# Kernel optimization log

Measured on AMD Instinct MI355X. Metric: run time of the kernel, lower is better.

## Reference

```python
import jax, jax.numpy as jnp
import numpy as np

TEMPERATURE = 0.5
N_NODES = 100000
N_EDGES = 3200000
D = 32


def setup_inputs() -> dict:
    key = jax.random.key(0)
    ks = jax.random.split(key, 8)
    node_reps = jax.random.normal(ks[0], (N_NODES, D), dtype=jnp.float32)
    edge_reps = jax.random.normal(ks[1], (N_EDGES, D), dtype=jnp.float32)
    graph_rep = jax.random.normal(ks[2], (D,), dtype=jnp.float32)
    subgraph_rep = jax.random.normal(ks[3], (D,), dtype=jnp.float32)
    W = jax.random.normal(ks[4], (3 * D, D), dtype=jnp.float32) / np.sqrt(3 * D)
    b = jax.random.normal(ks[5], (D,), dtype=jnp.float32) * 0.01
    edge_index = jax.random.randint(ks[6], (2, N_EDGES), 0, N_NODES, dtype=jnp.int64)
    selection = jax.random.randint(ks[7], (N_EDGES,), 0, 2) > 0
    return {
        "node_reps": node_reps,
        "edge_reps": edge_reps,
        "graph_rep": graph_rep,
        "subgraph_rep": subgraph_rep,
        "W": W,
        "b": b,
        "edge_index": edge_index,
        "selection": selection,
    }


def reference(node_reps, edge_reps, graph_rep, subgraph_rep, W, b, edge_index, selection):
    # Gather endpoint node reps per edge: [E, 32] each
    src = node_reps[edge_index[0]]
    dst = node_reps[edge_index[1]]
    # Concat -> [E, 96], Linear + ELU -> [E, 32]
    h = jnp.concatenate([src, dst, edge_reps], axis=1)
    edge_action_reps = jax.nn.elu(h @ W + b)
    # State scores: [E] = [E,32] @ [32]
    state_prob = edge_action_reps @ (graph_rep - subgraph_rep)
    # Mask already-selected edges to the global minimum, then softmax with temperature
    min_prob = jnp.min(state_prob)
    state_prob = jnp.where(selection, min_prob, state_prob)
    return jax.nn.softmax(state_prob[None, :] / TEMPERATURE, axis=1)
```

## Files before the change

### kernel.cpp

```cpp
#include <hip/hip_runtime.h>
#include <hip/hip_bf16.h>
#include <stdint.h>

#define DD 32
#define KH 96


typedef __attribute__((ext_vector_type(16))) float vf16;

__device__ __forceinline__ uint32_t fkey(float f) {
    uint32_t b = __float_as_uint(f);
    return (b & 0x80000000u) ? ~b : (b | 0x80000000u);
}
__device__ __forceinline__ float funkey(uint32_t k) {
    uint32_t b = (k & 0x80000000u) ? (k & 0x7FFFFFFFu) : ~k;
    return __uint_as_float(b);
}
__device__ __forceinline__ float bflo(uint32_t w) { return __uint_as_float(w << 16); }
__device__ __forceinline__ float bfhi(uint32_t w) { return __uint_as_float(w & 0xFFFF0000u); }
__device__ __forceinline__ uint16_t f2bf(float v) {
    uint32_t u = __float_as_uint(v);
    uint32_t r = (u + 0x7FFFu + ((u >> 16) & 1u)) >> 16;
    return (uint16_t)r;
}

__device__ __forceinline__ void wload(const float* p, vf16& a, vf16& b) {
    asm volatile("s_load_dwordx16 %0, %2, 0x0\n\t"
                 "s_load_dwordx16 %1, %2, 0x40\n\t"
                 "s_waitcnt lgkmcnt(0)"
                 : "=&s"(a), "=&s"(b)
                 : "s"(p));
}

__global__ void k_init(const void* W, const void* bias, const void* g, const void* sg,
                       const void* ei, const void* sel,
                       uint32_t* hdr, float* Wf, float* bf, float* vf, int E, int N) {
    int t = threadIdx.x;
    __shared__ int sh_i32, sh_gt1, sh_odd, sh_f32;
    if (t == 0) { sh_i32 = 0; sh_gt1 = 0; sh_odd = 0; sh_f32 = 0; }
    __syncthreads();

    const uint16_t* wb = (const uint16_t*)W;
    for (int i = t; i < KH * DD; i += 256) {
        float x = bflo((uint32_t)wb[i]);
        if (!(fabsf(x) < 1e4f)) sh_f32 = 1;
    }
    const long long* ell = (const long long*)ei;
    int ns = 2048 < E ? 2048 : E;
    for (int i = t; i < ns; i += 256) {
        long long v = ell[i];
        if (v < 0 || v >= (long long)N) sh_i32 = 1;
    }
    const uint32_t* sw = (const uint32_t*)sel;
    int ns2 = 2048 < E / 4 ? 2048 : E / 4;
    for (int i = t; i < ns2; i += 256) {
        uint32_t v = sw[i];
        if (v > 1u) sh_gt1 = 1;
        if (v != 0u && (i & 1)) sh_odd = 1;
    }
    __syncthreads();
    int fmode = sh_f32;

    for (int i = t; i < KH * DD; i += 256)
        Wf[i] = fmode ? ((const float*)W)[i] : bflo((uint32_t)wb[i]);
    for (int i = t; i < DD; i += 256) {
        bf[i] = fmode ? ((const float*)bias)[i] : bflo((uint32_t)((const uint16_t*)bias)[i]);
        float gv = fmode ? ((const float*)g)[i]  : bflo((uint32_t)((const uint16_t*)g)[i]);
        float sv = fmode ? ((const float*)sg)[i] : bflo((uint32_t)((const uint16_t*)sg)[i]);
        vf[i] = gv - sv;
    }
    if (t == 0) {
        hdr[0] = (uint32_t)sh_i32;
        hdr[1] = sh_gt1 ? 2u : (sh_odd ? 1u : 0u);
        hdr[2] = (uint32_t)fmode;
        hdr[3] = 0xFFFFFFFFu;
        hdr[4] = 0u;
        hdr[5] = 0u;
        hdr[6] = 0u;
    }
}

__device__ __forceinline__ void loadrow(const char* __restrict__ p, int fmode, float* h) {
    if (fmode) {
        const float4* q = (const float4*)p;
        #pragma unroll
        for (int t = 0; t < 8; ++t) {
            float4 u = q[t];
            h[t * 4 + 0] = u.x; h[t * 4 + 1] = u.y; h[t * 4 + 2] = u.z; h[t * 4 + 3] = u.w;
        }
    } else {
        const uint4* q = (const uint4*)p;
        #pragma unroll
        for (int t = 0; t < 4; ++t) {
            uint4 u = q[t];
            h[t * 8 + 0] = bflo(u.x); h[t * 8 + 1] = bfhi(u.x);
            h[t * 8 + 2] = bflo(u.y); h[t * 8 + 3] = bfhi(u.y);
            h[t * 8 + 4] = bflo(u.z); h[t * 8 + 5] = bfhi(u.z);
            h[t * 8 + 6] = bflo(u.w); h[t * 8 + 7] = bfhi(u.w);
        }
    }
}

__device__ __forceinline__ bool fetch_sel(const char* sel, int mode, int e) {
    if (mode == 2) return ((const uint8_t*)sel)[e] != 0;
    if (mode == 1) return ((const int*)sel)[e] != 0;
    return ((const long long*)sel)[e] != 0;
}

__device__ __forceinline__ void sp_store(float* __restrict__ ws_sp, void* __restrict__ out,
                                         int use_ws, int fmode, int e, float v) {
    if (use_ws) ws_sp[e] = v;
    else if (fmode) ((float*)out)[e] = v;
    else ((uint16_t*)out)[e] = f2bf(v);
}
__device__ __forceinline__ float sp_load(const float* __restrict__ ws_sp, const void* __restrict__ out,
                                         int use_ws, int fmode, int e) {
    if (use_ws) return ws_sp[e];
    if (fmode) return ((const float*)out)[e];
    return bflo((uint32_t)((const uint16_t*)out)[e]);
}

__global__ __launch_bounds__(256) void k_pass1(
    const char* __restrict__ node, const char* __restrict__ edgep,
    const char* __restrict__ ei, const char* __restrict__ sel,
    uint32_t* __restrict__ hdr, const float* __restrict__ Wf,
    const float* __restrict__ bf, const float* __restrict__ vf,
    float* __restrict__ ws_sp, void* __restrict__ out,
    int use_ws, int E, int N) {
    const int idx_mode = (int)hdr[0];
    const int sel_mode = (int)hdr[1];
    const int fmode    = (int)hdr[2];

    int e = blockIdx.x * 256 + threadIdx.x;
    bool valid = e < E;
    int ec = valid ? e : E - 1;

    long long si, di;
    if (idx_mode) { si = ((const int*)ei)[ec]; di = ((const int*)ei)[E + ec]; }
    else          { si = ((const long long*)ei)[ec]; di = ((const long long*)ei)[(size_t)E + ec]; }
    int s0 = (int)si; s0 = s0 < 0 ? 0 : (s0 >= N ? N - 1 : s0);
    int d0 = (int)di; d0 = d0 < 0 ? 0 : (d0 >= N ? N - 1 : d0);

    size_t rb = fmode ? 128 : 64;
    const char* p0 = node  + (size_t)s0 * rb;
    const char* p1 = node  + (size_t)d0 * rb;
    const char* p2 = edgep + (size_t)ec * rb;

    float acc[DD];
    {
        vf16 b0, b1;
        wload(bf, b0, b1);
        #pragma unroll
        for (int j = 0; j < 16; ++j) { acc[j] = b0[j]; acc[16 + j] = b1[j]; }
    }

    float hh[32], hn[32];
    loadrow(p0, fmode, hh);

    #pragma unroll 1
    for (int r = 0; r < 3; ++r) {
        if (r < 2) {
            const char* pn = (r == 0) ? p1 : p2;
            loadrow(pn, fmode, hn);
        }
        const float* wp = Wf + r * 32 * DD;
        #pragma unroll
        for (int k = 0; k < 32; ++k) {
            vf16 w0, w1;
            wload(wp + k * DD, w0, w1);
            float hk = hh[k];
            #pragma unroll
            for (int j = 0; j < 16; ++j) {
                acc[j]      = fmaf(hk, w0[j], acc[j]);
                acc[16 + j] = fmaf(hk, w1[j], acc[16 + j]);
            }
        }
        if (r < 2) {
            #pragma unroll
            for (int k = 0; k < 32; ++k) hh[k] = hn[k];
        }
    }

    float sp = 0.f;
    {
        vf16 v0, v1;
        wload(vf, v0, v1);
        #pragma unroll
        for (int j = 0; j < 16; ++j) {
            float a = acc[j];
            float act = a > 0.f ? a : (__expf(a) - 1.f);
            sp = fmaf(act, v0[j], sp);
            float a2 = acc[16 + j];
            float act2 = a2 > 0.f ? a2 : (__expf(a2) - 1.f);
            sp = fmaf(act2, v1[j], sp);
        }
    }

    bool selv = true;
    if (valid) {
        sp_store(ws_sp, out, use_ws, fmode, e, sp);
        selv = fetch_sel(sel, sel_mode, e);
    }

    float mn = valid ? sp : __builtin_inff();
    float mx = (valid && !selv) ? sp : -__builtin_inff();
    uint32_t c = (valid && !selv) ? 1u : 0u;
    #pragma unroll
    for (int o = 32; o >= 1; o >>= 1) {
        mn = fminf(mn, __shfl_xor(mn, o));
        mx = fmaxf(mx, __shfl_xor(mx, o));
        c += __shfl_xor(c, o);
    }
    __shared__ float smn[4], smx[4];
    __shared__ uint32_t sc[4];
    int wid = threadIdx.x >> 6, lane = threadIdx.x & 63;
    if (lane == 0) { smn[wid] = mn; smx[wid] = mx; sc[wid] = c; }
    __syncthreads();
    if (threadIdx.x == 0) {
        for (int w = 1; w < 4; ++w) { mn = fminf(mn, smn[w]); mx = fmaxf(mx, smx[w]); c += sc[w]; }
        atomicMin(&hdr[3], fkey(mn));
        atomicMax(&hdr[4], fkey(mx));
        if (c) atomicAdd(&hdr[5], c);
    }
}

__global__ __launch_bounds__(256) void k_pass2(
    const char* __restrict__ sel, uint32_t* __restrict__ hdr,
    const float* __restrict__ ws_sp, const void* __restrict__ out,
    int use_ws, int E) {
    int e = blockIdx.x * 256 + threadIdx.x;
    int sel_mode = (int)hdr[1], fmode = (int)hdr[2];
    float mn = funkey(hdr[3]);
    uint32_t cnt = hdr[5];
    float M = cnt ? funkey(hdr[4]) : mn;
    float p = 0.f;
    if (e < E) {
        float sp = sp_load(ws_sp, out, use_ws, fmode, e);
        bool selv = fetch_sel(sel, sel_mode, e);
        float masked = selv ? mn : sp;
        p = __expf((masked - M) * 2.0f);
    }
    #pragma unroll
    for (int o = 32; o >= 1; o >>= 1) p += __shfl_xor(p, o);
    __shared__ float sps[4];
    int wid = threadIdx.x >> 6, lane = threadIdx.x & 63;
    if (lane == 0) sps[wid] = p;
    __syncthreads();
    if (threadIdx.x == 0) {
        p += sps[1] + sps[2] + sps[3];
        atomicAdd((float*)&hdr[6], p);
    }
}

__global__ __launch_bounds__(256) void k_pass3(
    const char* __restrict__ sel, const uint32_t* __restrict__ hdr,
    const float* __restrict__ ws_sp, void* __restrict__ out,
    int use_ws, int E) {
    int e = blockIdx.x * 256 + threadIdx.x;
    if (e >= E) return;
    int sel_mode = (int)hdr[1], fmode = (int)hdr[2];
    float mn = funkey(hdr[3]);
    uint32_t cnt = hdr[5];
    float M = cnt ? funkey(hdr[4]) : mn;
    float S = __uint_as_float(hdr[6]);
    float sp = sp_load(ws_sp, out, use_ws, fmode, e);
    bool selv = fetch_sel(sel, sel_mode, e);
    float masked = selv ? mn : sp;
    float r = __expf((masked - M) * 2.0f) / S;
    if (fmode) ((float*)out)[e] = r;
    else       ((uint16_t*)out)[e] = f2bf(r);
}

extern "C" void kernel_launch(void* const* d_in, const int* in_sizes, int n_in,
                              void* d_out, int out_size, void* d_ws, size_t ws_size,
                              hipStream_t stream) {
    int N = in_sizes[0] / DD;
    int E = in_sizes[1] / DD;
    const void* node = d_in[0];
    const void* edge = d_in[1];
    const void* g    = d_in[2];
    const void* sg   = d_in[3];
    const void* W    = d_in[4];
    const void* bias = d_in[5];
    const void* ei   = d_in[6];
    const void* sel  = d_in[7];

    uint8_t* ws = (uint8_t*)d_ws;
    uint32_t* hdr = (uint32_t*)ws;
    float* Wf = (float*)(ws + 256);
    float* bf = (float*)(ws + 256 + 12288);
    float* vf = (float*)(ws + 256 + 12288 + 128);
    float* sp_arr = (float*)(ws + 16384);
    int use_ws = (ws_size >= (size_t)16384 + (size_t)E * sizeof(float)) ? 1 : 0;

    int grid = (E + 255) / 256;
    k_init<<<1, 256, 0, stream>>>(W, bias, g, sg, ei, sel, hdr, Wf, bf, vf, E, N);
    k_pass1<<<grid, 256, 0, stream>>>((const char*)node, (const char*)edge, (const char*)ei,
                                      (const char*)sel, hdr, Wf, bf, vf, sp_arr, d_out,
                                      use_ws, E, N);
    k_pass2<<<grid, 256, 0, stream>>>((const char*)sel, hdr, sp_arr, d_out, use_ws, E);
    k_pass3<<<grid, 256, 0, stream>>>((const char*)sel, hdr, sp_arr, d_out, use_ws, E);
}
```

Measured before the change: 1.131 ms.

## Stream weights via vector loads with triple-buffer prefetch; grid-stride all passes

Swaps the scalar s_load weight fetches, each of which waited on its own load, for per-thread float4 vector loads of W. These are triple-buffered two rows ahead so the loads overlap the FMAs, which are written as explicit v_fmac inline asm. All three passes become grid-stride loops with capped grids (2048 blocks for pass1, 1024 for passes 2 and 3), which cuts the per-block atomics and reduction overhead. Launch bounds now ask for 2 blocks per SIMD. The risks are higher VGPR pressure from the 24 float4 weight registers, and redundant per-lane vector loads of data that is uniform across the wave.

```diff
diff --git a/kernel.cpp b/kernel.cpp
--- a/kernel.cpp
+++ b/kernel.cpp
@@ -5,8 +5,6 @@
 #define DD 32
 #define KH 96
 
-
-typedef __attribute__((ext_vector_type(16))) float vf16;
 
 __device__ __forceinline__ uint32_t fkey(float f) {
     uint32_t b = __float_as_uint(f);
@@ -24,13 +22,7 @@
     return (uint16_t)r;
 }
 
-__device__ __forceinline__ void wload(const float* p, vf16& a, vf16& b) {
-    asm volatile("s_load_dwordx16 %0, %2, 0x0\n\t"
-                 "s_load_dwordx16 %1, %2, 0x40\n\t"
-                 "s_waitcnt lgkmcnt(0)"
-                 : "=&s"(a), "=&s"(b)
-                 : "s"(p));
-}
+#define VFMAC(d, a, b) asm("v_fmac_f32 %0, %1, %2" : "+v"(d) : "v"(a), "v"(b))
 
 __global__ void k_init(const void* W, const void* bias, const void* g, const void* sg,
                        const void* ei, const void* sel,
@@ -120,7 +112,26 @@
     return bflo((uint32_t)((const uint16_t*)out)[e]);
 }
 
-__global__ __launch_bounds__(256) void k_pass1(
+#define RSEC(R)                                                             \
+    _Pragma("unroll")                                                       \
+    for (int k = 0; k < 32; ++k) {                                          \
+        const int g = (R) * 32 + k;                                         \
+        if (g + 2 < 96) {                                                   \
+            _Pragma("unroll")                                               \
+            for (int q = 0; q < 8; ++q) w[(g + 2) % 3][q] = wq[(g + 2) * 8 + q]; \
+        }                                                                   \
+        float hk = hh[k];                                                   \
+        _Pragma("unroll")                                                   \
+        for (int q = 0; q < 8; ++q) {                                       \
+            float4 c4 = w[g % 3][q];                                        \
+            VFMAC(acc[q * 4 + 0], hk, c4.x);                                \
+            VFMAC(acc[q * 4 + 1], hk, c4.y);                                \
+            VFMAC(acc[q * 4 + 2], hk, c4.z);                                \
+            VFMAC(acc[q * 4 + 3], hk, c4.w);                                \
+        }                                                                   \
+    }
+
+__global__ __launch_bounds__(256, 2) void k_pass1(
     const char* __restrict__ node, const char* __restrict__ edgep,
     const char* __restrict__ ei, const char* __restrict__ sel,
     uint32_t* __restrict__ hdr, const float* __restrict__ Wf,
@@ -131,80 +142,78 @@
     const int sel_mode = (int)hdr[1];
     const int fmode    = (int)hdr[2];
 
-    int e = blockIdx.x * 256 + threadIdx.x;
-    bool valid = e < E;
-    int ec = valid ? e : E - 1;
-
-    long long si, di;
-    if (idx_mode) { si = ((const int*)ei)[ec]; di = ((const int*)ei)[E + ec]; }
-    else          { si = ((const long long*)ei)[ec]; di = ((const long long*)ei)[(size_t)E + ec]; }
-    int s0 = (int)si; s0 = s0 < 0 ? 0 : (s0 >= N ? N - 1 : s0);
-    int d0 = (int)di; d0 = d0 < 0 ? 0 : (d0 >= N ? N - 1 : d0);
-
-    size_t rb = fmode ? 128 : 64;
-    const char* p0 = node  + (size_t)s0 * rb;
-    const char* p1 = node  + (size_t)d0 * rb;
-    const char* p2 = edgep + (size_t)ec * rb;
-
-    float acc[DD];
-    {
-        vf16 b0, b1;
-        wload(bf, b0, b1);
-        #pragma unroll
-        for (int j = 0; j < 16; ++j) { acc[j] = b0[j]; acc[16 + j] = b1[j]; }
-    }
-
-    float hh[32], hn[32];
-    loadrow(p0, fmode, hh);
-
-    #pragma unroll 1
-    for (int r = 0; r < 3; ++r) {
-        if (r < 2) {
-            const char* pn = (r == 0) ? p1 : p2;
-            loadrow(pn, fmode, hn);
-        }
-        const float* wp = Wf + r * 32 * DD;
-        #pragma unroll
-        for (int k = 0; k < 32; ++k) {
-            vf16 w0, w1;
-            wload(wp + k * DD, w0, w1);
-            float hk = hh[k];
-            #pragma unroll
-            for (int j = 0; j < 16; ++j) {
-                acc[j]      = fmaf(hk, w0[j], acc[j]);
-                acc[16 + j] = fmaf(hk, w1[j], acc[16 + j]);
-            }
-        }
-        if (r < 2) {
-            #pragma unroll
-            for (int k = 0; k < 32; ++k) hh[k] = hn[k];
-        }
-    }
-
-    float sp = 0.f;
-    {
-        vf16 v0, v1;
-        wload(vf, v0, v1);
+    const float4* __restrict__ wq = (const float4*)Wf;
+    const float4* __restrict__ bq = (const float4*)bf;
+    const float4* __restrict__ vq = (const float4*)vf;
+
+    float mnA = __builtin_inff();
+    float mxA = -__builtin_inff();
+    uint32_t cA = 0;
+
+    const int stride = gridDim.x * 256;
+    for (int e = blockIdx.x * 256 + threadIdx.x; e < E; e += stride) {
+        long long si, di;
+        if (idx_mode) { si = ((const int*)ei)[e]; di = ((const int*)ei)[E + e]; }
+        else          { si = ((const long long*)ei)[e]; di = ((const long long*)ei)[(size_t)E + e]; }
+        int s0 = (int)si; s0 = s0 < 0 ? 0 : (s0 >= N ? N - 1 : s0);
+        int d0 = (int)di; d0 = d0 < 0 ? 0 : (d0 >= N ? N - 1 : d0);
+
+        size_t rb = fmode ? 128 : 64;
+        const char* p0 = node  + (size_t)s0 * rb;
+        const char* p1 = node  + (size_t)d0 * rb;
+        const char* p2 = edgep + (size_t)e * rb;
+
+        float hh[DD];
+        loadrow(p0, fmode, hh);
+
+        float acc[DD];
+        #pragma unroll
+        for (int q = 0; q < 8; ++q) {
+            float4 b4 = bq[q];
+            acc[q * 4 + 0] = b4.x; acc[q * 4 + 1] = b4.y;
+            acc[q * 4 + 2] = b4.z; acc[q * 4 + 3] = b4.w;
+        }
+
+        float4 w[3][8];
+        #pragma unroll
+        for (int q = 0; q < 8; ++q) w[0][q] = wq[q];
+        #pragma unroll
+        for (int q = 0; q < 8; ++q) w[1][q] = wq[8 + q];
+
+        RSEC(0)
+        loadrow(p1, fmode, hh);
+        RSEC(1)
+        loadrow(p2, fmode, hh);
+        RSEC(2)
+
+        float vv[DD];
+        #pragma unroll
+        for (int q = 0; q < 8; ++q) {
+            float4 v4 = vq[q];
+            vv[q * 4 + 0] = v4.x; vv[q * 4 + 1] = v4.y;
+            vv[q * 4 + 2] = v4.z; vv[q * 4 + 3] = v4.w;
+        }
+        float sp = 0.f;
         #pragma unroll
         for (int j = 0; j < 16; ++j) {
             float a = acc[j];
             float act = a > 0.f ? a : (__expf(a) - 1.f);
-            sp = fmaf(act, v0[j], sp);
+            sp = fmaf(act, vv[j], sp);
             float a2 = acc[16 + j];
             float act2 = a2 > 0.f ? a2 : (__expf(a2) - 1.f);
-            sp = fmaf(act2, v1[j], sp);
-        }
-    }
-
-    bool selv = true;
-    if (valid) {
+            sp = fmaf(act2, vv[16 + j], sp);
+        }
+
         sp_store(ws_sp, out, use_ws, fmode, e, sp);
-        selv = fetch_sel(sel, sel_mode, e);
-    }
-
-    float mn = valid ? sp : __builtin_inff();
-    float mx = (valid && !selv) ? sp : -__builtin_inff();
-    uint32_t c = (valid && !selv) ? 1u : 0u;
+        bool selv = fetch_sel(sel, sel_mode, e);
+
+        mnA = fminf(mnA, sp);
+        mxA = selv ? mxA : fmaxf(mxA, sp);
+        cA += selv ? 0u : 1u;
+    }
+
+    float mn = mnA, mx = mxA;
+    uint32_t c = cA;
     #pragma unroll
     for (int o = 32; o >= 1; o >>= 1) {
         mn = fminf(mn, __shfl_xor(mn, o));
@@ -217,7 +226,7 @@
     if (lane == 0) { smn[wid] = mn; smx[wid] = mx; sc[wid] = c; }
     __syncthreads();
     if (threadIdx.x == 0) {
-        for (int w = 1; w < 4; ++w) { mn = fminf(mn, smn[w]); mx = fmaxf(mx, smx[w]); c += sc[w]; }
+        for (int w2 = 1; w2 < 4; ++w2) { mn = fminf(mn, smn[w2]); mx = fmaxf(mx, smx[w2]); c += sc[w2]; }
         atomicMin(&hdr[3], fkey(mn));
         atomicMax(&hdr[4], fkey(mx));
         if (c) atomicAdd(&hdr[5], c);
@@ -228,17 +237,18 @@
     const char* __restrict__ sel, uint32_t* __restrict__ hdr,
     const float* __restrict__ ws_sp, const void* __restrict__ out,
     int use_ws, int E) {
-    int e = blockIdx.x * 256 + threadIdx.x;
     int sel_mode = (int)hdr[1], fmode = (int)hdr[2];
     float mn = funkey(hdr[3]);
     uint32_t cnt = hdr[5];
     float M = cnt ? funkey(hdr[4]) : mn;
+
     float p = 0.f;
-    if (e < E) {
+    const int stride = gridDim.x * 256;
+    for (int e = blockIdx.x * 256 + threadIdx.x; e < E; e += stride) {
         float sp = sp_load(ws_sp, out, use_ws, fmode, e);
         bool selv = fetch_sel(sel, sel_mode, e);
         float masked = selv ? mn : sp;
-        p = __expf((masked - M) * 2.0f);
+        p += __expf((masked - M) * 2.0f);
     }
     #pragma unroll
     for (int o = 32; o >= 1; o >>= 1) p += __shfl_xor(p, o);
@@ -256,19 +266,20 @@
     const char* __restrict__ sel, const uint32_t* __restrict__ hdr,
     const float* __restrict__ ws_sp, void* __restrict__ out,
     int use_ws, int E) {
-    int e = blockIdx.x * 256 + threadIdx.x;
-    if (e >= E) return;
     int sel_mode = (int)hdr[1], fmode = (int)hdr[2];
     float mn = funkey(hdr[3]);
     uint32_t cnt = hdr[5];
     float M = cnt ? funkey(hdr[4]) : mn;
     float S = __uint_as_float(hdr[6]);
-    float sp = sp_load(ws_sp, out, use_ws, fmode, e);
-    bool selv = fetch_sel(sel, sel_mode, e);
-    float masked = selv ? mn : sp;
-    float r = __expf((masked - M) * 2.0f) / S;
-    if (fmode) ((float*)out)[e] = r;
-    else       ((uint16_t*)out)[e] = f2bf(r);
+    const int stride = gridDim.x * 256;
+    for (int e = blockIdx.x * 256 + threadIdx.x; e < E; e += stride) {
+        float sp = sp_load(ws_sp, out, use_ws, fmode, e);
+        bool selv = fetch_sel(sel, sel_mode, e);
+        float masked = selv ? mn : sp;
+        float r = __expf((masked - M) * 2.0f) / S;
+        if (fmode) ((float*)out)[e] = r;
+        else       ((uint16_t*)out)[e] = f2bf(r);
+    }
 }
 
 extern "C" void kernel_launch(void* const* d_in, const int* in_sizes, int n_in,
@@ -293,11 +304,14 @@
     float* sp_arr = (float*)(ws + 16384);
     int use_ws = (ws_size >= (size_t)16384 + (size_t)E * sizeof(float)) ? 1 : 0;
 
-    int grid = (E + 255) / 256;
+    int full = (E + 255) / 256;
+    int grid1 = full < 2048 ? full : 2048;
+    int grid23 = full < 1024 ? full : 1024;
+
     k_init<<<1, 256, 0, stream>>>(W, bias, g, sg, ei, sel, hdr, Wf, bf, vf, E, N);
-    k_pass1<<<grid, 256, 0, stream>>>((const char*)node, (const char*)edge, (const char*)ei,
-                                      (const char*)sel, hdr, Wf, bf, vf, sp_arr, d_out,
-                                      use_ws, E, N);
-    k_pass2<<<grid, 256, 0, stream>>>((const char*)sel, hdr, sp_arr, d_out, use_ws, E);
-    k_pass3<<<grid, 256, 0, stream>>>((const char*)sel, hdr, sp_arr, d_out, use_ws, E);
-}
+    k_pass1<<<grid1, 256, 0, stream>>>((const char*)node, (const char*)edge, (const char*)ei,
+                                       (const char*)sel, hdr, Wf, bf, vf, sp_arr, d_out,
+                                       use_ws, E, N);
+    k_pass2<<<grid23, 256, 0, stream>>>((const char*)sel, hdr, sp_arr, d_out, use_ws, E);
+    k_pass3<<<grid23, 256, 0, stream>>>((const char*)sel, hdr, sp_arr, d_out, use_ws, E);
+}
```

After: 1.043 ms. 7.8% less time.
